# Performance work log

Hardware: AMD Instinct MI355X
Metric: run time of the kernel (lower is better)

## Reference

```python
import jax, jax.numpy as jnp
import numpy as np

B, T, N = 16, 1024, 128
WIN, STEP = 30, 2
MOMENT_ORDERS = (2, 4, 8)
D_MODEL = 256


def _mask_diag(corr):
    n = corr.shape[-1]
    eye = jnp.eye(n, dtype=corr.dtype)
    return corr * (1.0 - eye) + eye


def corrcoef_time(xw):
    # xw: [..., L, N] -> corr over channels: [..., N, N]
    L = xw.shape[-2]
    xm = xw - xw.mean(axis=-2, keepdims=True)
    cov = jnp.einsum('...ln,...lm->...nm', xm, xm) / (L - 1 + 1e-8)
    var = jnp.clip(jnp.diagonal(cov, axis1=-2, axis2=-1), 1e-8, None)
    std = jnp.sqrt(var)
    corr = cov / (std[..., :, None] * std[..., None, :])
    corr = jnp.nan_to_num(corr, nan=0.0, posinf=0.0, neginf=0.0)
    return _mask_diag(corr)


def rowwise_corr(M):
    # M: [B, N, F]
    Xc = M - M.mean(axis=-1, keepdims=True)
    num = jnp.einsum('bnf,bmf->bnm', Xc, Xc)
    den1 = jnp.sqrt(jnp.clip((Xc ** 2).sum(axis=-1), 1e-8, None))
    corr = num / (den1[:, :, None] * den1[:, None, :])
    corr = jnp.nan_to_num(corr, nan=0.0, posinf=0.0, neginf=0.0)
    return _mask_diag(corr)


def layer_norm(x, gamma, beta, eps=1e-5):
    mu = x.mean(axis=-1, keepdims=True)
    var = ((x - mu) ** 2).mean(axis=-1, keepdims=True)
    return (x - mu) / jnp.sqrt(var + eps) * gamma + beta


def normalize_adj(adj):
    n = adj.shape[-1]
    A_hat = adj + jnp.eye(n, dtype=adj.dtype)
    d = A_hat.sum(axis=-1)
    dis = jnp.sqrt(1.0 / jnp.clip(d, 1e-8, None))
    return A_hat * dis[:, :, None] * dis[:, None, :]


def setup_inputs() -> dict:
    key = jax.random.key(0)
    ks = jax.random.split(key, 8)
    in_dim = len(MOMENT_ORDERS) * N
    return {
        'x': jax.random.normal(ks[0], (B, T, N), dtype=jnp.float32),
        'ln_gamma': jnp.ones((in_dim,), jnp.float32),
        'ln_beta': jnp.zeros((in_dim,), jnp.float32),
        'W1': jax.random.normal(ks[1], (in_dim, D_MODEL), jnp.float32) * 0.05,
        'b1': jnp.zeros((D_MODEL,), jnp.float32),
        'W2': jax.random.normal(ks[2], (D_MODEL, D_MODEL), jnp.float32) * 0.05,
        'b2': jnp.zeros((D_MODEL,), jnp.float32),
        'Wc': jax.random.normal(ks[3], (D_MODEL, 1), jnp.float32) * 0.05,
        'bc': jnp.zeros((1,), jnp.float32),
    }


def reference(x, ln_gamma, ln_beta, W1, b1, W2, b2, Wc, bc):
    # sliding windows (static indices)
    starts = np.arange(0, T - WIN + 1, STEP)
    idx = starts[:, None] + np.arange(WIN)[None, :]
    xw = x[:, idx, :]
    lo = corrcoef_time(xw)                            # [B, Wn, N, N]

    mean_lo = lo.mean(axis=1, keepdims=True)
    centered = lo - mean_lo
    cm_list, ho_list = [], []
    for d in MOMENT_ORDERS:
        cm = jnp.nan_to_num((centered ** d).mean(axis=1),
                            nan=0.0, posinf=0.0, neginf=0.0)  # [B, N, N]
        cm_list.append(cm)
        ho_list.append(rowwise_corr(cm))

    X = jnp.concatenate(cm_list, axis=-1)             # [B, N, 3N]
    X = layer_norm(X, ln_gamma, ln_beta)

    A = jnp.stack(ho_list, axis=1).mean(axis=1)
    A = 0.5 * (A + jnp.swapaxes(A, 1, 2))
    A_norm = normalize_adj(A)

    H = jax.nn.relu(jnp.einsum('bnm,bmd->bnd', A_norm, X @ W1 + b1))
    H = jax.nn.relu(jnp.einsum('bnm,bmd->bnd', A_norm, H @ W2 + b2))
    g = H.mean(axis=1)                                # [B, d_model]
    out = jax.nn.sigmoid(g @ Wc + bc)                 # [B, 1]
    return out
```

## Files before the change

### kernel.cpp

```cpp
#include <hip/hip_runtime.h>
#include <math.h>

#define BB  16
#define TT  1024
#define NN  128
#define WIN 30
#define NWD 498
#define DM  256
#define IND 384
#define GW  16

#define INV_W (1.0f/498.0f)

#define SARR (BB*NN*NN)

#define OFF_A     0
#define OFF_G     (OFF_A    + BB*NWD*NN)
#define OFF_CM2   (OFF_G    + BB*NWD*NN)
#define OFF_CM4   (OFF_CM2  + SARR)
#define OFF_CM8   (OFF_CM4  + SARR)
#define OFF_AD    (OFF_CM8  + SARR)
#define OFF_PART  (OFF_AD   + 3*SARR)
#define OFF_ANORM OFF_PART
#define OFF_BUFA  (OFF_ANORM + SARR)
#define OFF_BUFB  (OFF_BUFA + BB*NN*DM)
#define OFF_CTR   (OFF_PART + 768*16384)
#define OFF_GW1   OFF_A
#define OFF_SG    (OFF_GW1 + IND*DM)
#define OFF_SB    (OFF_SG  + DM)

#define GLL16(gsrc, ldst) \
    __builtin_amdgcn_global_load_lds((const __attribute__((address_space(1))) void*)(gsrc), \
                                     (__attribute__((address_space(3))) void*)(ldst), 16, 0, 0)

__global__ __launch_bounds__(128) void k1_stats(const float* __restrict__ x, float* __restrict__ ws) {
    int bx = blockIdx.x;
    if (bx == 0 && threadIdx.x < 128) ((unsigned*)(ws + OFF_CTR))[threadIdx.x] = 0u;
    int c = bx & 15, b = bx >> 4;
    int w0 = c*32, w1 = min(NWD, w0+32);
    int n = threadIdx.x;
    const float* xp = x + (size_t)b*TT*NN + n;

    float sum = 0.f, sq = 0.f;
    for (int t = 2*w0; t < 2*w0 + WIN; ++t) {
        float v = xp[(size_t)t*NN];
        sum += v; sq = fmaf(v, v, sq);
    }
    for (int w = w0; w < w1; ++w) {
        if (w > w0) {
            float o0 = xp[(size_t)(2*w-2)*NN], o1 = xp[(size_t)(2*w-1)*NN];
            float n0 = xp[(size_t)(2*w+28)*NN], n1 = xp[(size_t)(2*w+29)*NN];
            sum += (n0 + n1) - (o0 + o1);
            sq  += (n0*n0 + n1*n1) - (o0*o0 + o1*o1);
        }
        float mean = sum * (1.0f/30.0f);
        float ss = sq - 30.0f*mean*mean;
        float var = fmaxf(ss * (1.0f/29.0f), 1e-8f);
        float a = (1.0f / sqrtf(var)) * 0.185695338f;
        ws[OFF_A + ((size_t)b*NWD + w)*NN + n] = a;
        ws[OFF_G + ((size_t)b*NWD + w)*NN + n] = mean * a * 5.477225575f;
    }
}

__global__ __launch_bounds__(256) __attribute__((amdgpu_waves_per_eu(3, 3)))
void k24_inc(const float* __restrict__ x, float* __restrict__ ws) {
    __shared__ __align__(16) float xr[64][NN];
    __shared__ __align__(16) float sa[GW][NN];
    __shared__ __align__(16) float sg[GW][NN];
    int bx = blockIdx.x;
    int wc = bx & 7;
    int slab = (bx >> 3) % 6;
    int b = bx / 48;
    const char IS[6] = {0,0,0,0,1,1};
    const char JS[6] = {0,1,2,3,2,3};
    int is = IS[slab], js = JS[slab];
    int w0 = wc * 63, w1 = min(NWD, w0 + 63);
    int tid = threadIdx.x;
    int jg = tid & 7, ig = tid >> 3;
    int i0 = is*64 + ig*2;
    int j0 = js*32 + jg*4;

    const float* xb = x + (size_t)b*TT*NN;
    const float* Ab = ws + OFF_A + (size_t)b*NWD*NN;
    const float* Gb = ws + OFF_G + (size_t)b*NWD*NN;

    float P[2][4];
    float S1[2][4], S2[2][4], S3[2][4], S4[2][4], S5[2][4], S6[2][4], S7[2][4], S8[2][4];
#pragma unroll
    for (int p=0;p<2;++p)
#pragma unroll
        for (int q=0;q<4;++q) {
            P[p][q]=0.f;
            S1[p][q]=0.f;S2[p][q]=0.f;S3[p][q]=0.f;S4[p][q]=0.f;
            S5[p][q]=0.f;S6[p][q]=0.f;S7[p][q]=0.f;S8[p][q]=0.f;
        }

    auto moments = [&](int k) {
        float2 ai = *(const float2*)&sa[k][i0];
        float2 gi = *(const float2*)&sg[k][i0];
        float4 aj = *(const float4*)&sa[k][j0];
        float4 gj = *(const float4*)&sg[k][j0];
        float av[2] = {ai.x, ai.y};
        float mg[2] = {-gi.x, -gi.y};
        float aw[4] = {aj.x, aj.y, aj.z, aj.w};
        float gw[4] = {gj.x, gj.y, gj.z, gj.w};
#pragma unroll
        for (int p=0;p<2;++p)
#pragma unroll
            for (int q=0;q<4;++q) {
                float aa  = av[p]*aw[q];
                float ngg = mg[p]*gw[q];
                float c   = fmaf(P[p][q], aa, ngg);
                float c2 = c*c;
                float c3 = c2*c;
                float c4 = c2*c2;
                S1[p][q] += c;
                S2[p][q] += c2;
                S3[p][q] += c3;
                S4[p][q] += c4;
                S5[p][q] = fmaf(c4, c,  S5[p][q]);
                S6[p][q] = fmaf(c3, c3, S6[p][q]);
                S7[p][q] = fmaf(c3, c4, S7[p][q]);
                S8[p][q] = fmaf(c4, c4, S8[p][q]);
            }
    };

    int rlo = 2*w0;
    for (int wg = w0; wg < w1; wg += GW) {
        int m = min(GW, w1 - wg);
        __syncthreads();
        int rhi = 2*(wg + m - 1) + 29;
        int nr = rhi - rlo + 1;
        for (int idx = tid; idx < nr*32; idx += 256) {
            int r = idx >> 5, c4 = idx & 31;
            int t = rlo + r;
            GLL16(xb + (size_t)t*NN + c4*4, &xr[t & 63][c4*4]);
        }
        for (int idx = tid; idx < m*32; idx += 256) {
            int k = idx >> 5, c4 = idx & 31;
            GLL16(Ab + (size_t)(wg+k)*NN + c4*4, &sa[k][c4*4]);
        }
        for (int idx = tid; idx < m*32; idx += 256) {
            int k = idx >> 5, c4 = idx & 31;
            GLL16(Gb + (size_t)(wg+k)*NN + c4*4, &sg[k][c4*4]);
        }
        rlo = rhi + 1;
        __syncthreads();

        int kstart = 0;
        if (wg == w0) {
#pragma unroll 6
            for (int k = 0; k < WIN; ++k) {
                int t = 2*w0 + k;
                float2 xi = *(const float2*)&xr[t & 63][i0];
                float4 xj = *(const float4*)&xr[t & 63][j0];
                float av[2] = {xi.x, xi.y};
                float bv[4] = {xj.x, xj.y, xj.z, xj.w};
#pragma unroll
                for (int p=0;p<2;++p)
#pragma unroll
                    for (int q=0;q<4;++q) P[p][q] = fmaf(av[p], bv[q], P[p][q]);
            }
            moments(0);
            kstart = 1;
        }
        for (int k = kstart; k < m; ++k) {
            int w = wg + k;
            int tr[4] = {2*w - 2, 2*w - 1, 2*w + 28, 2*w + 29};
#pragma unroll
            for (int kk = 0; kk < 4; ++kk) {
                int t = tr[kk];
                float sgn = (kk < 2) ? -1.0f : 1.0f;
                float2 xi = *(const float2*)&xr[t & 63][i0];
                float4 xj = *(const float4*)&xr[t & 63][j0];
                float av[2] = {sgn*xi.x, sgn*xi.y};
                float bv[4] = {xj.x, xj.y, xj.z, xj.w};
#pragma unroll
                for (int p=0;p<2;++p)
#pragma unroll
                    for (int q=0;q<4;++q) P[p][q] = fmaf(av[p], bv[q], P[p][q]);
            }
            moments(k);
        }
    }

    float* tp = ws + OFF_PART + (size_t)bx*16384 + tid*8;
#define STORE_ARR(A, S) \
    *(float4*)&tp[(A)*2048]     = make_float4(S[0][0], S[0][1], S[0][2], S[0][3]); \
    *(float4*)&tp[(A)*2048 + 4] = make_float4(S[1][0], S[1][1], S[1][2], S[1][3]);
    STORE_ARR(0, S1) STORE_ARR(1, S2) STORE_ARR(2, S3) STORE_ARR(3, S4)
    STORE_ARR(4, S5) STORE_ARR(5, S6) STORE_ARR(6, S7) STORE_ARR(7, S8)
#undef STORE_ARR
}

__global__ __launch_bounds__(256) void kred(const float* __restrict__ gamma, const float* __restrict__ beta,
                                            const float* __restrict__ W1, float* __restrict__ ws) {
    int bxg = blockIdx.x;
    int tid = threadIdx.x;
    if (bxg >= 768) {
        int gi = bxg - 768;
        if (gi < 96) {
#pragma unroll
            for (int kk = 0; kk < 4; ++kk) {
                int k = gi*4 + kk;
                ws[OFF_GW1 + (size_t)k*DM + tid] = gamma[k] * W1[(size_t)k*DM + tid];
            }
        } else {
            float sgv = 0.f, sbv = 0.f;
            for (int k = 0; k < IND; ++k) {
                float w = W1[(size_t)k*DM + tid];
                sgv = fmaf(gamma[k], w, sgv);
                sbv = fmaf(beta[k],  w, sbv);
            }
            ws[OFF_SG + tid] = sgv;
            ws[OFF_SB + tid] = sbv;
        }
        return;
    }
    int pair = bxg >> 3, sub = bxg & 7;
    int b = pair / 6, slab = pair % 6;
    const char IS[6] = {0,0,0,0,1,1};
    const char JS[6] = {0,1,2,3,2,3};
    int is = IS[slab], js = JS[slab];
    int off = sub*256 + tid;
    const float* base = ws + OFF_PART + (size_t)(b*48 + slab*8)*16384;

    float E[8];
#pragma unroll
    for (int a=0;a<8;++a) E[a] = 0.f;
    for (int c = 0; c < 8; ++c) {
        const float* tp = base + (size_t)c*16384;
#pragma unroll
        for (int a=0;a<8;++a) E[a] += tp[a*2048 + off];
    }

    int tid_old = off >> 3, e = off & 7;
    int ig = tid_old >> 3, jg = tid_old & 7;
    int p = e >> 2, q = e & 3;
    int i = is*64 + ig*2 + p;
    int j = js*32 + jg*4 + q;

    float cm2, cm4, cm8;
    if (i == j) {
        cm2 = 0.f; cm4 = 0.f; cm8 = 0.f;
    } else {
        float e1 = E[0]*INV_W, e2 = E[1]*INV_W, e3 = E[2]*INV_W, e4 = E[3]*INV_W;
        float e5 = E[4]*INV_W, e6 = E[5]*INV_W, e7 = E[6]*INV_W, e8 = E[7]*INV_W;
        float m  = e1;
        float m2 = m*m, m3 = m2*m, m4 = m2*m2, m5 = m4*m, m6 = m3*m3, m8 = m4*m4;
        cm2 = e2 - m2;
        cm4 = e4 - 4.f*m*e3 + 6.f*m2*e2 - 3.f*m4;
        cm8 = e8 - 8.f*m*e7 + 28.f*m2*e6 - 56.f*m3*e5 + 70.f*m4*e4
                 - 56.f*m5*e3 + 28.f*m6*e2 - 7.f*m8;
    }
    float* C2 = ws + OFF_CM2 + (size_t)b*NN*NN;
    float* C4 = ws + OFF_CM4 + (size_t)b*NN*NN;
    float* C8 = ws + OFF_CM8 + (size_t)b*NN*NN;
    C2[i*NN + j] = cm2; C2[j*NN + i] = cm2;
    C4[i*NN + j] = cm4; C4[j*NN + i] = cm4;
    C8[i*NN + j] = cm8; C8[j*NN + i] = cm8;
}

#define XSTR 132
__global__ __launch_bounds__(256) void kB(const float* __restrict__ b1, float* __restrict__ ws) {
    __shared__ __align__(16) float smem[64*XSTR + 2*NN];
    __shared__ unsigned winB;
    int blk = blockIdx.x, tid = threadIdx.x;
    if (blk < 192) {
        int rem = blk % 12;
        int b = blk / 12, di = rem >> 2, jq = rem & 3;
        float* Xct = smem;
        float* Mr  = smem + 64*XSTR;
        float* Ir  = Mr + NN;
        const float* cm = ws + (di==0 ? OFF_CM2 : (di==1 ? OFF_CM4 : OFF_CM8)) + (size_t)b*NN*NN;
        int n0 = (tid >> 4)*8, m0 = jq*32 + (tid & 15)*2;
        float s1 = 0.f, s2 = 0.f;
        float acc0[8], acc1[8];
#pragma unroll
        for (int k=0;k<8;++k) { acc0[k]=0.f; acc1[k]=0.f; }

        for (int h = 0; h < 2; ++h) {
            __syncthreads();
            for (int idx = tid; idx < NN*64; idx += 256) {
                int n = idx >> 6, f0 = idx & 63;
                Xct[f0*XSTR + n] = cm[n*NN + h*64 + f0];
            }
            __syncthreads();
            if (tid < NN) {
                for (int f0 = 0; f0 < 64; ++f0) {
                    float v = Xct[f0*XSTR + tid];
                    s1 += v; s2 = fmaf(v, v, s2);
                }
            }
            for (int f0 = 0; f0 < 64; ++f0) {
                const float* row = &Xct[f0*XSTR];
                float4 a0 = *(const float4*)&row[n0];
                float4 a1 = *(const float4*)&row[n0+4];
                float2 bm = *(const float2*)&row[m0];
                float av[8] = {a0.x,a0.y,a0.z,a0.w,a1.x,a1.y,a1.z,a1.w};
#pragma unroll
                for (int k=0;k<8;++k) {
                    acc0[k] = fmaf(av[k], bm.x, acc0[k]);
                    acc1[k] = fmaf(av[k], bm.y, acc1[k]);
                }
            }
        }
        __syncthreads();
        if (tid < NN) {
            float mean = s1 * (1.0f/NN);
            Mr[tid] = mean;
            Ir[tid] = 1.0f/sqrtf(fmaxf(s2 - (float)NN*mean*mean, 1e-8f));
        }
        __syncthreads();
        float rm0 = Mr[m0], rm1 = Mr[m0+1], im0 = Ir[m0], im1 = Ir[m0+1];
        float* Ad = ws + OFF_AD + (size_t)(b*3 + di)*NN*NN;
#pragma unroll
        for (int k=0;k<8;++k) {
            int gi = n0+k;
            float rn = Mr[gi], inv = Ir[gi];
            float v0 = (acc0[k] - (float)NN*rn*rm0) * inv * im0;
            float v1 = (acc1[k] - (float)NN*rn*rm1) * inv * im1;
            if (gi == m0)   v0 = 1.0f;
            if (gi == m0+1) v1 = 1.0f;
            Ad[gi*NN + m0]     = v0;
            Ad[gi*NN + m0 + 1] = v1;
        }

        __syncthreads();
        if (tid == 0) {
            unsigned* ctr = (unsigned*)(ws + OFF_CTR);
            unsigned old = __hip_atomic_fetch_add(&ctr[96 + b], 1u,
                                                  __ATOMIC_ACQ_REL, __HIP_MEMORY_SCOPE_AGENT);
            winB = (old == 11u) ? 1u : 0u;
        }
        __syncthreads();
        if (winB) {
            float* dis = smem;
            const float* A0 = ws + OFF_AD + (size_t)(b*3 + 0)*NN*NN;
            const float* A1 = ws + OFF_AD + (size_t)(b*3 + 1)*NN*NN;
            const float* A2 = ws + OFF_AD + (size_t)(b*3 + 2)*NN*NN;
            if (tid < NN) {
                float d = 1.0f;
                for (int m = 0; m < NN; ++m) {
                    int o = tid*NN + m;
                    d += (A0[o] + A1[o] + A2[o]) * (1.0f/3.0f);
                }
                dis[tid] = sqrtf(1.0f / fmaxf(d, 1e-8f));
            }
            __syncthreads();
            float* An = ws + OFF_ANORM + (size_t)b*NN*NN;
            for (int idx = tid; idx < NN*NN; idx += 256) {
                int n = idx >> 7, m = idx & 127;
                float s = (A0[idx] + A1[idx] + A2[idx]) * (1.0f/3.0f);
                float v = s + (n==m ? 1.0f : 0.0f);
                An[idx] = v * dis[n] * dis[m];
            }
        }
    } else {
        int r0 = (blk - 192) * 4;
        float* sms = smem;
        float* srs = smem + 4;
        {
            int rloc = tid >> 6, lane = tid & 63;
            int grow = r0 + rloc;
            int b = grow >> 7, n = grow & 127;
            const float* c2 = ws + OFF_CM2 + ((size_t)b*NN + n)*NN;
            const float* c4 = ws + OFF_CM4 + ((size_t)b*NN + n)*NN;
            const float* c8 = ws + OFF_CM8 + ((size_t)b*NN + n)*NN;
            float s1 = 0.f, s2 = 0.f;
            for (int e = lane; e < IND; e += 64) {
                float v = (e < 128) ? c2[e] : (e < 256) ? c4[e-128] : c8[e-256];
                s1 += v; s2 = fmaf(v, v, s2);
            }
#pragma unroll
            for (int o = 32; o > 0; o >>= 1) {
                s1 += __shfl_down(s1, o, 64);
                s2 += __shfl_down(s2, o, 64);
            }
            if (lane == 0) {
                float mean = s1 * (1.0f/IND);
                sms[rloc] = mean;
                srs[rloc] = 1.0f / sqrtf(s2*(1.0f/IND) - mean*mean + 1e-5f);
            }
        }
        __syncthreads();
        float mean[4], rstd[4];
        const float* xrow[4];
#pragma unroll
        for (int r = 0; r < 4; ++r) {
            mean[r] = sms[r]; rstd[r] = srs[r];
        }
        float acc[4] = {0.f, 0.f, 0.f, 0.f};
        const float* GW1p = ws + OFF_GW1;
#pragma unroll
        for (int seg = 0; seg < 3; ++seg) {
            int offc = (seg==0) ? OFF_CM2 : (seg==1) ? OFF_CM4 : OFF_CM8;
#pragma unroll
            for (int r = 0; r < 4; ++r) {
                int grow = r0 + r;
                xrow[r] = ws + offc + ((size_t)(grow >> 7)*NN + (grow & 127))*NN;
            }
            const float* gseg = GW1p + (size_t)(seg*128)*DM + tid;
            for (int k = 0; k < 128; k += 2) {
                float g0 = gseg[(size_t)(k+0)*DM];
                float g1 = gseg[(size_t)(k+1)*DM];
#pragma unroll
                for (int r = 0; r < 4; ++r) {
                    acc[r] = fmaf(xrow[r][k+0], g0, acc[r]);
                    acc[r] = fmaf(xrow[r][k+1], g1, acc[r]);
                }
            }
        }
        float sgv = ws[OFF_SG + tid];
        float sbb = ws[OFF_SB + tid] + b1[tid];
        float* O = ws + OFF_BUFA;
#pragma unroll
        for (int r = 0; r < 4; ++r)
            O[(size_t)(r0+r)*DM + tid] = rstd[r]*(acc[r] - mean[r]*sgv) + sbb;
    }
}

__global__ __launch_bounds__(256) void k98_propgemm(const float* __restrict__ W2, const float* __restrict__ b2,
                                                    const float* __restrict__ An, const float* __restrict__ Zin,
                                                    float* __restrict__ Out) {
    __shared__ float Hs[8][DM];
    int bx = blockIdx.x;
    int b = bx >> 4, n0 = (bx & 15)*8;
    int tid = threadIdx.x;
    const float* A = An + (size_t)b*NN*NN + (size_t)n0*NN;
    const float* Z = Zin + (size_t)b*NN*DM;
    float acc[8] = {0,0,0,0,0,0,0,0};
    for (int m = 0; m < NN; m += 4) {
        float z0 = Z[(size_t)(m+0)*DM + tid];
        float z1 = Z[(size_t)(m+1)*DM + tid];
        float z2 = Z[(size_t)(m+2)*DM + tid];
        float z3 = Z[(size_t)(m+3)*DM + tid];
#pragma unroll
        for (int r = 0; r < 8; ++r) {
            const float* Ar = A + r*NN + m;
            acc[r] = fmaf(Ar[0], z0, acc[r]);
            acc[r] = fmaf(Ar[1], z1, acc[r]);
            acc[r] = fmaf(Ar[2], z2, acc[r]);
            acc[r] = fmaf(Ar[3], z3, acc[r]);
        }
    }
#pragma unroll
    for (int r = 0; r < 8; ++r) Hs[r][tid] = fmaxf(acc[r], 0.0f);
    __syncthreads();
    float acc2[8];
    float bv = b2[tid];
#pragma unroll
    for (int r = 0; r < 8; ++r) acc2[r] = bv;
    for (int k = 0; k < DM; k += 4) {
        float w0 = W2[(size_t)(k+0)*DM + tid];
        float w1 = W2[(size_t)(k+1)*DM + tid];
        float w2 = W2[(size_t)(k+2)*DM + tid];
        float w3 = W2[(size_t)(k+3)*DM + tid];
#pragma unroll
        for (int r = 0; r < 8; ++r) {
            float4 h = *(const float4*)&Hs[r][k];
            acc2[r] = fmaf(h.x, w0, acc2[r]);
            acc2[r] = fmaf(h.y, w1, acc2[r]);
            acc2[r] = fmaf(h.z, w2, acc2[r]);
            acc2[r] = fmaf(h.w, w3, acc2[r]);
        }
    }
    float* O = Out + (size_t)b*NN*DM;
#pragma unroll
    for (int r = 0; r < 8; ++r) O[(size_t)(n0+r)*DM + tid] = acc2[r];
}

__global__ __launch_bounds__(256) void k9_prop(const float* __restrict__ Wc, const float* __restrict__ bc,
                                               const float* __restrict__ An, const float* __restrict__ Zin,
                                               float* __restrict__ Out,
                                               float* __restrict__ ws, float* __restrict__ outp) {
    __shared__ float red[256];
    __shared__ unsigned win9;
    int bx = blockIdx.x;
    int b = bx >> 4, n0 = (bx & 15)*8;
    int tid = threadIdx.x;
    const float* A = An + (size_t)b*NN*NN + (size_t)n0*NN;
    const float* Z = Zin + (size_t)b*NN*DM;
    float acc[8] = {0,0,0,0,0,0,0,0};
    for (int m = 0; m < NN; m += 4) {
        float z0 = Z[(size_t)(m+0)*DM + tid];
        float z1 = Z[(size_t)(m+1)*DM + tid];
        float z2 = Z[(size_t)(m+2)*DM + tid];
        float z3 = Z[(size_t)(m+3)*DM + tid];
#pragma unroll
        for (int r = 0; r < 8; ++r) {
            const float* Ar = A + r*NN + m;
            acc[r] = fmaf(Ar[0], z0, acc[r]);
            acc[r] = fmaf(Ar[1], z1, acc[r]);
            acc[r] = fmaf(Ar[2], z2, acc[r]);
            acc[r] = fmaf(Ar[3], z3, acc[r]);
        }
    }
    float* O = Out + (size_t)b*NN*DM;
#pragma unroll
    for (int r = 0; r < 8; ++r) O[(size_t)(n0+r)*DM + tid] = fmaxf(acc[r], 0.0f);

    __syncthreads();
    if (tid == 0) {
        unsigned* ctr = (unsigned*)(ws + OFF_CTR);
        unsigned old = __hip_atomic_fetch_add(&ctr[112 + b], 1u,
                                              __ATOMIC_ACQ_REL, __HIP_MEMORY_SCOPE_AGENT);
        win9 = (old == 15u) ? 1u : 0u;
    }
    __syncthreads();
    if (win9) {
        const float* H = Out + (size_t)b*NN*DM;
        float s = 0.f;
        for (int n = 0; n < NN; ++n) s += H[(size_t)n*DM + tid];
        red[tid] = s * (1.0f/NN) * Wc[tid];
        __syncthreads();
        for (int o = 128; o > 0; o >>= 1) { if (tid < o) red[tid] += red[tid+o]; __syncthreads(); }
        if (tid == 0) outp[b] = 1.0f/(1.0f + expf(-(red[0] + bc[0])));
    }
}

extern "C" void kernel_launch(void* const* d_in, const int* in_sizes, int n_in,
                              void* d_out, int out_size, void* d_ws, size_t ws_size,
                              hipStream_t stream) {
    (void)in_sizes; (void)n_in; (void)out_size; (void)ws_size;
    const float* x     = (const float*)d_in[0];
    const float* gamma = (const float*)d_in[1];
    const float* beta  = (const float*)d_in[2];
    const float* W1    = (const float*)d_in[3];
    const float* b1    = (const float*)d_in[4];
    const float* W2    = (const float*)d_in[5];
    const float* b2    = (const float*)d_in[6];
    const float* Wc    = (const float*)d_in[7];
    const float* bc    = (const float*)d_in[8];
    float* ws  = (float*)d_ws;
    float* out = (float*)d_out;

    k1_stats    <<<BB*16,    128, 0, stream>>>(x, ws);
    k24_inc     <<<BB*6*8,   256, 0, stream>>>(x, ws);
    kred        <<<768+96+1, 256, 0, stream>>>(gamma, beta, W1, ws);
    kB          <<<704,      256, 0, stream>>>(b1, ws);
    k98_propgemm<<<BB*16,    256, 0, stream>>>(W2, b2, ws + OFF_ANORM, ws + OFF_BUFA, ws + OFF_BUFB);
    k9_prop     <<<BB*16,    256, 0, stream>>>(Wc, bc, ws + OFF_ANORM, ws + OFF_BUFB, ws + OFF_BUFA, ws, out);
}
```

Measured before the change: 233.5 us.

## Vectorize partial-moment reduction, halve propagation row tiles, shrink k24 window group

The reduction kernel now reads partial moment sums as float4, with each thread handling four adjacent output columns. This cuts the grid from 768 to 192 reduction blocks and lowers the per-thread index arithmetic. The two graph-propagation kernels now use 4 rows per block instead of 8, doubling their grid to 512 blocks for better CU occupancy, and the completion counter threshold is updated to match. k24_inc uses a smaller window group (GW 8) and targets 4 waves per EU, trading register budget for occupancy and possibly causing spills.

After: 238.5 us. 1.02x slower.

```diff
diff --git a/kernel.cpp b/kernel.cpp
--- a/kernel.cpp
+++ b/kernel.cpp
@@ -8,7 +8,7 @@
 #define NWD 498
 #define DM  256
 #define IND 384
-#define GW  16
+#define GW  8
 
 #define INV_W (1.0f/498.0f)
 
@@ -62,7 +62,7 @@
     }
 }
 
-__global__ __launch_bounds__(256) __attribute__((amdgpu_waves_per_eu(3, 3)))
+__global__ __launch_bounds__(256) __attribute__((amdgpu_waves_per_eu(4, 4)))
 void k24_inc(const float* __restrict__ x, float* __restrict__ ws) {
     __shared__ __align__(16) float xr[64][NN];
     __shared__ __align__(16) float sa[GW][NN];
@@ -197,8 +197,8 @@
                                             const float* __restrict__ W1, float* __restrict__ ws) {
     int bxg = blockIdx.x;
     int tid = threadIdx.x;
-    if (bxg >= 768) {
-        int gi = bxg - 768;
+    if (bxg >= 192) {
+        int gi = bxg - 192;
         if (gi < 96) {
 #pragma unroll
             for (int kk = 0; kk < 4; ++kk) {
@@ -217,48 +217,56 @@
         }
         return;
     }
-    int pair = bxg >> 3, sub = bxg & 7;
+    int pair = bxg >> 1, half = bxg & 1;
     int b = pair / 6, slab = pair % 6;
     const char IS[6] = {0,0,0,0,1,1};
     const char JS[6] = {0,1,2,3,2,3};
     int is = IS[slab], js = JS[slab];
-    int off = sub*256 + tid;
-    const float* base = ws + OFF_PART + (size_t)(b*48 + slab*8)*16384;
-
-    float E[8];
-#pragma unroll
-    for (int a=0;a<8;++a) E[a] = 0.f;
+    int off4 = half*256 + tid;
+    const float4* base = (const float4*)(ws + OFF_PART + (size_t)(b*48 + slab*8)*16384);
+
+    float4 E[8];
+#pragma unroll
+    for (int a=0;a<8;++a) E[a] = make_float4(0.f,0.f,0.f,0.f);
     for (int c = 0; c < 8; ++c) {
-        const float* tp = base + (size_t)c*16384;
-#pragma unroll
-        for (int a=0;a<8;++a) E[a] += tp[a*2048 + off];
-    }
-
-    int tid_old = off >> 3, e = off & 7;
+        const float4* tp = base + (size_t)c*4096;
+#pragma unroll
+        for (int a=0;a<8;++a) {
+            float4 v = tp[a*512 + off4];
+            E[a].x += v.x; E[a].y += v.y; E[a].z += v.z; E[a].w += v.w;
+        }
+    }
+    float Es[8][4];
+#pragma unroll
+    for (int a=0;a<8;++a) { Es[a][0]=E[a].x; Es[a][1]=E[a].y; Es[a][2]=E[a].z; Es[a][3]=E[a].w; }
+
+    int tid_old = off4 >> 1, p = off4 & 1;
     int ig = tid_old >> 3, jg = tid_old & 7;
-    int p = e >> 2, q = e & 3;
-    int i = is*64 + ig*2 + p;
-    int j = js*32 + jg*4 + q;
-
-    float cm2, cm4, cm8;
-    if (i == j) {
-        cm2 = 0.f; cm4 = 0.f; cm8 = 0.f;
-    } else {
-        float e1 = E[0]*INV_W, e2 = E[1]*INV_W, e3 = E[2]*INV_W, e4 = E[3]*INV_W;
-        float e5 = E[4]*INV_W, e6 = E[5]*INV_W, e7 = E[6]*INV_W, e8 = E[7]*INV_W;
-        float m  = e1;
-        float m2 = m*m, m3 = m2*m, m4 = m2*m2, m5 = m4*m, m6 = m3*m3, m8 = m4*m4;
-        cm2 = e2 - m2;
-        cm4 = e4 - 4.f*m*e3 + 6.f*m2*e2 - 3.f*m4;
-        cm8 = e8 - 8.f*m*e7 + 28.f*m2*e6 - 56.f*m3*e5 + 70.f*m4*e4
-                 - 56.f*m5*e3 + 28.f*m6*e2 - 7.f*m8;
-    }
+    int i  = is*64 + ig*2 + p;
+    int j0 = js*32 + jg*4;
     float* C2 = ws + OFF_CM2 + (size_t)b*NN*NN;
     float* C4 = ws + OFF_CM4 + (size_t)b*NN*NN;
     float* C8 = ws + OFF_CM8 + (size_t)b*NN*NN;
-    C2[i*NN + j] = cm2; C2[j*NN + i] = cm2;
-    C4[i*NN + j] = cm4; C4[j*NN + i] = cm4;
-    C8[i*NN + j] = cm8; C8[j*NN + i] = cm8;
+#pragma unroll
+    for (int l = 0; l < 4; ++l) {
+        int j = j0 + l;
+        float cm2, cm4, cm8;
+        if (i == j) {
+            cm2 = 0.f; cm4 = 0.f; cm8 = 0.f;
+        } else {
+            float e1 = Es[0][l]*INV_W, e2 = Es[1][l]*INV_W, e3 = Es[2][l]*INV_W, e4 = Es[3][l]*INV_W;
+            float e5 = Es[4][l]*INV_W, e6 = Es[5][l]*INV_W, e7 = Es[6][l]*INV_W, e8 = Es[7][l]*INV_W;
+            float m  = e1;
+            float m2 = m*m, m3 = m2*m, m4 = m2*m2, m5 = m4*m, m6 = m3*m3, m8 = m4*m4;
+            cm2 = e2 - m2;
+            cm4 = e4 - 4.f*m*e3 + 6.f*m2*e2 - 3.f*m4;
+            cm8 = e8 - 8.f*m*e7 + 28.f*m2*e6 - 56.f*m3*e5 + 70.f*m4*e4
+                     - 56.f*m5*e3 + 28.f*m6*e2 - 7.f*m8;
+        }
+        C2[i*NN + j] = cm2; C2[j*NN + i] = cm2;
+        C4[i*NN + j] = cm4; C4[j*NN + i] = cm4;
+        C8[i*NN + j] = cm8; C8[j*NN + i] = cm8;
+    }
 }
 
 #define XSTR 132
@@ -423,20 +431,20 @@
 __global__ __launch_bounds__(256) void k98_propgemm(const float* __restrict__ W2, const float* __restrict__ b2,
                                                     const float* __restrict__ An, const float* __restrict__ Zin,
                                                     float* __restrict__ Out) {
-    __shared__ float Hs[8][DM];
+    __shared__ float Hs[4][DM];
     int bx = blockIdx.x;
-    int b = bx >> 4, n0 = (bx & 15)*8;
+    int b = bx >> 5, n0 = (bx & 31)*4;
     int tid = threadIdx.x;
     const float* A = An + (size_t)b*NN*NN + (size_t)n0*NN;
     const float* Z = Zin + (size_t)b*NN*DM;
-    float acc[8] = {0,0,0,0,0,0,0,0};
+    float acc[4] = {0,0,0,0};
     for (int m = 0; m < NN; m += 4) {
         float z0 = Z[(size_t)(m+0)*DM + tid];
         float z1 = Z[(size_t)(m+1)*DM + tid];
         float z2 = Z[(size_t)(m+2)*DM + tid];
         float z3 = Z[(size_t)(m+3)*DM + tid];
 #pragma unroll
-        for (int r = 0; r < 8; ++r) {
+        for (int r = 0; r < 4; ++r) {
             const float* Ar = A + r*NN + m;
             acc[r] = fmaf(Ar[0], z0, acc[r]);
             acc[r] = fmaf(Ar[1], z1, acc[r]);
@@ -445,19 +453,19 @@
         }
     }
 #pragma unroll
-    for (int r = 0; r < 8; ++r) Hs[r][tid] = fmaxf(acc[r], 0.0f);
+    for (int r = 0; r < 4; ++r) Hs[r][tid] = fmaxf(acc[r], 0.0f);
     __syncthreads();
-    float acc2[8];
+    float acc2[4];
     float bv = b2[tid];
 #pragma unroll
-    for (int r = 0; r < 8; ++r) acc2[r] = bv;
+    for (int r = 0; r < 4; ++r) acc2[r] = bv;
     for (int k = 0; k < DM; k += 4) {
         float w0 = W2[(size_t)(k+0)*DM + tid];
         float w1 = W2[(size_t)(k+1)*DM + tid];
         float w2 = W2[(size_t)(k+2)*DM + tid];
         float w3 = W2[(size_t)(k+3)*DM + tid];
 #pragma unroll
-        for (int r = 0; r < 8; ++r) {
+        for (int r = 0; r < 4; ++r) {
             float4 h = *(const float4*)&Hs[r][k];
             acc2[r] = fmaf(h.x, w0, acc2[r]);
             acc2[r] = fmaf(h.y, w1, acc2[r]);
@@ -467,7 +475,7 @@
     }
     float* O = Out + (size_t)b*NN*DM;
 #pragma unroll
-    for (int r = 0; r < 8; ++r) O[(size_t)(n0+r)*DM + tid] = acc2[r];
+    for (int r = 0; r < 4; ++r) O[(size_t)(n0+r)*DM + tid] = acc2[r];
 }
 
 __global__ __launch_bounds__(256) void k9_prop(const float* __restrict__ Wc, const float* __restrict__ bc,
@@ -477,18 +485,18 @@
     __shared__ float red[256];
     __shared__ unsigned win9;
     int bx = blockIdx.x;
-    int b = bx >> 4, n0 = (bx & 15)*8;
+    int b = bx >> 5, n0 = (bx & 31)*4;
     int tid = threadIdx.x;
     const float* A = An + (size_t)b*NN*NN + (size_t)n0*NN;
     const float* Z = Zin + (size_t)b*NN*DM;
-    float acc[8] = {0,0,0,0,0,0,0,0};
+    float acc[4] = {0,0,0,0};
     for (int m = 0; m < NN; m += 4) {
         float z0 = Z[(size_t)(m+0)*DM + tid];
         float z1 = Z[(size_t)(m+1)*DM + tid];
         float z2 = Z[(size_t)(m+2)*DM + tid];
         float z3 = Z[(size_t)(m+3)*DM + tid];
 #pragma unroll
-        for (int r = 0; r < 8; ++r) {
+        for (int r = 0; r < 4; ++r) {
             const float* Ar = A + r*NN + m;
             acc[r] = fmaf(Ar[0], z0, acc[r]);
             acc[r] = fmaf(Ar[1], z1, acc[r]);
@@ -498,14 +506,14 @@
     }
     float* O = Out + (size_t)b*NN*DM;
 #pragma unroll
-    for (int r = 0; r < 8; ++r) O[(size_t)(n0+r)*DM + tid] = fmaxf(acc[r], 0.0f);
+    for (int r = 0; r < 4; ++r) O[(size_t)(n0+r)*DM + tid] = fmaxf(acc[r], 0.0f);
 
     __syncthreads();
     if (tid == 0) {
         unsigned* ctr = (unsigned*)(ws + OFF_CTR);
         unsigned old = __hip_atomic_fetch_add(&ctr[112 + b], 1u,
                                               __ATOMIC_ACQ_REL, __HIP_MEMORY_SCOPE_AGENT);
-        win9 = (old == 15u) ? 1u : 0u;
+        win9 = (old == 31u) ? 1u : 0u;
     }
     __syncthreads();
     if (win9) {
@@ -537,8 +545,8 @@
 
     k1_stats    <<<BB*16,    128, 0, stream>>>(x, ws);
     k24_inc     <<<BB*6*8,   256, 0, stream>>>(x, ws);
-    kred        <<<768+96+1, 256, 0, stream>>>(gamma, beta, W1, ws);
+    kred        <<<192+96+1, 256, 0, stream>>>(gamma, beta, W1, ws);
     kB          <<<704,      256, 0, stream>>>(b1, ws);
-    k98_propgemm<<<BB*16,    256, 0, stream>>>(W2, b2, ws + OFF_ANORM, ws + OFF_BUFA, ws + OFF_BUFB);
-    k9_prop     <<<BB*16,    256, 0, stream>>>(Wc, bc, ws + OFF_ANORM, ws + OFF_BUFB, ws + OFF_BUFA, ws, out);
-}
+    k98_propgemm<<<BB*32,    256, 0, stream>>>(W2, b2, ws + OFF_ANORM, ws + OFF_BUFA, ws + OFF_BUFB);
+    k9_prop     <<<BB*32,    256, 0, stream>>>(Wc, bc, ws + OFF_ANORM, ws + OFF_BUFB, ws + OFF_BUFA, ws, out);
+}
```
